# Optimization experiments

Hardware: AMD Instinct MI355X
Metric: run time of the kernel (lower is better)

## Reference

```python
import jax, jax.numpy as jnp
import numpy as np
from jax import lax

N_QUBITS = 4   # in_channels * kernel_size^2 = 1*2*2
N_LAYERS = 2
K = 2
STRIDE = 1


def _bshape(theta, N):
    # broadcast scalar or (N,) angle to (N, 1, 1, ..., 1) for statevector broadcasting
    return jnp.broadcast_to(theta, (N,)).reshape((N,) + (1,) * N_QUBITS)


def _rx(state, theta, w):
    # RX(theta) on wire w (axis w+1): cos(t/2) I - i sin(t/2) X
    N = state.shape[0]
    c = _bshape(jnp.cos(theta * 0.5), N)
    s = _bshape(jnp.sin(theta * 0.5), N)
    return c * state - 1j * s * jnp.flip(state, axis=w + 1)


def _rz(state, theta, w):
    # RZ(theta): phase e^{-i t/2} on |0>, e^{+i t/2} on |1> of wire w
    N = state.shape[0]
    sgn = jnp.array([-0.5, 0.5], dtype=state.real.dtype).reshape(
        (1,) * (w + 1) + (2,) + (1,) * (N_QUBITS - 1 - w))
    return state * jnp.exp(1j * (_bshape(theta, N) * sgn))


def _cnot(state, control, target):
    ca, ta = control + 1, target + 1
    s0 = jnp.take(state, 0, axis=ca)
    s1 = jnp.take(state, 1, axis=ca)
    ta2 = ta if ta < ca else ta - 1
    s1 = jnp.flip(s1, axis=ta2)
    return jnp.stack([s0, s1], axis=ca)


def _simulate(angles, params):
    # angles: (N, n_qubits) float32; params: (n_layers, n_qubits, 2)
    N = angles.shape[0]
    state = jnp.zeros((N,) + (2,) * N_QUBITS, dtype=jnp.complex64)
    state = state.at[(slice(None),) + (0,) * N_QUBITS].set(1.0)
    # AngleEmbedding: RX(x_w) on wire w
    for w in range(N_QUBITS):
        state = _rx(state, angles[:, w], w)
    # quantum_circuit_1
    for l in range(N_LAYERS):
        for w in range(N_QUBITS):
            state = _rx(state, params[l, w, 0], w)
            state = _rz(state, params[l, w, 1], w)
        for w in range(N_QUBITS - 1):
            # qml.CNOT(wires=[w+1, w]) -> control w+1, target w
            state = _cnot(state, w + 1, w)
    probs = state.real ** 2 + state.imag ** 2  # (N, 2,...,2)
    zs = []
    for w in range(N_QUBITS):
        other = tuple(a for a in range(1, N_QUBITS + 1) if a != w + 1)
        m = probs.sum(axis=other)  # (N, 2)
        zs.append(m[:, 0] - m[:, 1])
    return jnp.stack(zs, axis=1)  # (N, n_qubits)


def _forward(x, params):
    B, C, H, W = x.shape
    Ho = (H - K) // STRIDE + 1
    Wo = (W - K) // STRIDE + 1
    # (B, C*K*K, Ho, Wo); feature dim flattened channel-major (C, kh, kw),
    # matching torch.flatten(input[:, :, i:i+k, j:j+k], start_dim=1)
    patches = lax.conv_general_dilated_patches(x, (K, K), (STRIDE, STRIDE), 'VALID')
    angles = patches.transpose(0, 2, 3, 1).reshape(-1, N_QUBITS)  # (B*Ho*Wo, nq)
    z = _simulate(angles, params)  # (B*Ho*Wo, nq)
    return z.reshape(B, Ho, Wo, N_QUBITS).transpose(0, 3, 1, 2)  # (B, nq, Ho, Wo)


def setup_inputs() -> dict:
    key = jax.random.key(0)
    k1, k2 = jax.random.split(key)
    x = jax.random.uniform(k1, (32, 1, 128, 128), dtype=jnp.float32)
    params = jax.random.uniform(k2, (N_LAYERS, N_QUBITS, 2), dtype=jnp.float32)
    return {"x": x, "params": params}


def reference(x, params):
    return _forward(x, params)
```

## Files before the change

kernel.cpp:

```cpp
#include <hip/hip_runtime.h>


#define HH 128
#define WW 128
#define HO 127
#define WO 127
#define BB 32

template <int M>
__device__ __forceinline__ void rx_gate(float* re, float* im, float th) {
    float s, c;
    __sincosf(th * 0.5f, &s, &c);
#pragma unroll
    for (int idx = 0; idx < 16; ++idx) {
        if (idx & M) continue;
        const int p = idx | M;
        float r0 = re[idx], i0 = im[idx], r1 = re[p], i1 = im[p];
        re[idx] = fmaf(c, r0, s * i1);
        im[idx] = fmaf(c, i0, -s * r1);
        re[p]   = fmaf(c, r1, s * i0);
        im[p]   = fmaf(c, i1, -s * r0);
    }
}

template <int M>
__device__ __forceinline__ void rz_gate(float* re, float* im, float th) {
    float sp, cp;
    __sincosf(th * 0.5f, &sp, &cp);
#pragma unroll
    for (int idx = 0; idx < 16; ++idx) {
        float r = re[idx], q = im[idx];
        if (idx & M) {
            re[idx] = fmaf(r, cp, -q * sp);
            im[idx] = fmaf(q, cp, r * sp);
        } else {
            re[idx] = fmaf(r, cp, q * sp);
            im[idx] = fmaf(q, cp, -r * sp);
        }
    }
}

template <int CM, int TM>
__device__ __forceinline__ void cnot_gate(float* re, float* im) {
#pragma unroll
    for (int idx = 0; idx < 16; ++idx) {
        if ((idx & CM) && !(idx & TM)) {
            const int p = idx | TM;
            float t;
            t = re[idx]; re[idx] = re[p]; re[p] = t;
            t = im[idx]; im[idx] = im[p]; im[p] = t;
        }
    }
}

__global__ __launch_bounds__(256) void qconv_kernel(
    const float* __restrict__ x, const float* __restrict__ prm,
    float* __restrict__ out, int total) {
    int tid = blockIdx.x * blockDim.x + threadIdx.x;
    if (tid >= total) return;

    int j = tid % WO;
    int t = tid / WO;
    int i = t % HO;
    int b = t / HO;

    const float* xp = x + ((size_t)b * HH + i) * WW + j;
    float a0 = xp[0], a1 = xp[1], a2 = xp[WW], a3 = xp[WW + 1];

    float re[16], im[16];
#pragma unroll
    for (int k = 0; k < 16; ++k) { re[k] = 0.f; im[k] = 0.f; }
    re[0] = 1.0f;

    rx_gate<8>(re, im, a0);
    rx_gate<4>(re, im, a1);
    rx_gate<2>(re, im, a2);
    rx_gate<1>(re, im, a3);

#pragma unroll
    for (int l = 0; l < 2; ++l) {
        const float* p = prm + l * 8;
        rx_gate<8>(re, im, p[0]); rz_gate<8>(re, im, p[1]);
        rx_gate<4>(re, im, p[2]); rz_gate<4>(re, im, p[3]);
        rx_gate<2>(re, im, p[4]); rz_gate<2>(re, im, p[5]);
        rx_gate<1>(re, im, p[6]); rz_gate<1>(re, im, p[7]);
        cnot_gate<4, 8>(re, im);
        cnot_gate<2, 4>(re, im);
        cnot_gate<1, 2>(re, im);
    }

    float z0 = 0.f, z1 = 0.f, z2 = 0.f, z3 = 0.f;
#pragma unroll
    for (int idx = 0; idx < 16; ++idx) {
        float pr = fmaf(re[idx], re[idx], im[idx] * im[idx]);
        z0 += (idx & 8) ? -pr : pr;
        z1 += (idx & 4) ? -pr : pr;
        z2 += (idx & 2) ? -pr : pr;
        z3 += (idx & 1) ? -pr : pr;
    }

    float* o = out + (((size_t)b * 4) * HO + (size_t)i) * WO + j;
    o[0]            = z0;
    o[HO * WO]      = z1;
    o[2 * HO * WO]  = z2;
    o[3 * HO * WO]  = z3;
}

extern "C" void kernel_launch(void* const* d_in, const int* in_sizes, int n_in,
                              void* d_out, int out_size, void* d_ws, size_t ws_size,
                              hipStream_t stream) {
    const float* x = (const float*)d_in[0];
    const float* prm = (const float*)d_in[1];
    float* out = (float*)d_out;
    const int total = BB * HO * WO;
    const int blocks = (total + 255) / 256;
    qconv_kernel<<<blocks, 256, 0, stream>>>(x, prm, out, total);
}
```

Before: 75.19 us.

## Precompute Pauli-basis observable coefficients and evaluate as trig polynomial

Splits the work into a tiny setup kernel and an evaluation kernel. The setup kernel builds the 16x16 parameter unitary and expands each Z expectation into 81 coefficients over products of {1, sin, cos} of the input angles. The per-pixel kernel then evaluates that polynomial instead of simulating the full statevector through all the gates. This removes most per-thread arithmetic, but adds a second launch with a single-block serial setup and reads the coefficient table from workspace memory.

```diff
diff --git a/kernel.cpp b/kernel.cpp
--- a/kernel.cpp
+++ b/kernel.cpp
@@ -53,8 +53,80 @@
     }
 }
 
-__global__ __launch_bounds__(256) void qconv_kernel(
-    const float* __restrict__ x, const float* __restrict__ prm,
+__device__ __forceinline__ void param_circuit(float* re, float* im,
+                                              const float* __restrict__ prm) {
+#pragma unroll
+    for (int l = 0; l < 2; ++l) {
+        const float* p = prm + l * 8;
+        rx_gate<8>(re, im, p[0]); rz_gate<8>(re, im, p[1]);
+        rx_gate<4>(re, im, p[2]); rz_gate<4>(re, im, p[3]);
+        rx_gate<2>(re, im, p[4]); rz_gate<2>(re, im, p[5]);
+        rx_gate<1>(re, im, p[6]); rz_gate<1>(re, im, p[7]);
+        cnot_gate<4, 8>(re, im);
+        cnot_gate<2, 4>(re, im);
+        cnot_gate<1, 2>(re, im);
+    }
+}
+
+__global__ __launch_bounds__(384) void qconv_setup(const float* __restrict__ prm,
+                                                   float* __restrict__ W) {
+    __shared__ float Ur[16][16];
+    __shared__ float Ui[16][16];
+    const int tid = threadIdx.x;
+    if (tid < 16) {
+        float re[16], im[16];
+#pragma unroll
+        for (int k = 0; k < 16; ++k) { re[k] = (k == tid) ? 1.f : 0.f; im[k] = 0.f; }
+        param_circuit(re, im, prm);
+#pragma unroll
+        for (int k = 0; k < 16; ++k) { Ur[k][tid] = re[k]; Ui[k][tid] = im[k]; }
+    }
+    __syncthreads();
+    if (tid < 324) {
+        const int w = tid / 81;
+        int p = tid % 81;
+        const int t3 = p % 3; p /= 3;
+        const int t2 = p % 3; p /= 3;
+        const int t1 = p % 3;
+        const int t0 = p / 3;
+        const int f = (t0 == 1 ? 8 : 0) | (t1 == 1 ? 4 : 0) |
+                      (t2 == 1 ? 2 : 0) | (t3 == 1 ? 1 : 0);
+        const int zbit = 8 >> w;
+        float acc = 0.f;
+        for (int i = 0; i < 16; ++i) {
+            float pr = 1.f, pi = 0.f;
+            {
+                int ib;
+                ib = (i >> 3) & 1;
+                if (t0 == 2) { if (ib) { pr = -pr; pi = -pi; } }
+                else if (t0 == 1) { float tt = pr; if (ib) { pr = -pi; pi = tt; } else { pr = pi; pi = -tt; } }
+                ib = (i >> 2) & 1;
+                if (t1 == 2) { if (ib) { pr = -pr; pi = -pi; } }
+                else if (t1 == 1) { float tt = pr; if (ib) { pr = -pi; pi = tt; } else { pr = pi; pi = -tt; } }
+                ib = (i >> 1) & 1;
+                if (t2 == 2) { if (ib) { pr = -pr; pi = -pi; } }
+                else if (t2 == 1) { float tt = pr; if (ib) { pr = -pi; pi = tt; } else { pr = pi; pi = -tt; } }
+                ib = i & 1;
+                if (t3 == 2) { if (ib) { pr = -pr; pi = -pi; } }
+                else if (t3 == 1) { float tt = pr; if (ib) { pr = -pi; pi = tt; } else { pr = pi; pi = -tt; } }
+            }
+            const int j = i ^ f;
+            float sr = 0.f, si = 0.f;
+            for (int k = 0; k < 16; ++k) {
+                float zk = (k & zbit) ? -1.f : 1.f;
+                float ar = Ur[k][j], ai = Ui[k][j];
+                float br = Ur[k][i], bi = Ui[k][i];
+                sr += zk * fmaf(ar, br, ai * bi);
+                si += zk * fmaf(ar, bi, -ai * br);
+            }
+            acc += pr * sr - pi * si;
+        }
+        W[tid] = acc * (1.0f / 16.0f);
+    }
+}
+
+__global__ __launch_bounds__(256) void qconv_eval(
+    const float* __restrict__ x, const float* __restrict__ W,
     float* __restrict__ out, int total) {
     int tid = blockIdx.x * blockDim.x + threadIdx.x;
     if (tid >= total) return;
@@ -67,43 +139,48 @@
     const float* xp = x + ((size_t)b * HH + i) * WW + j;
     float a0 = xp[0], a1 = xp[1], a2 = xp[WW], a3 = xp[WW + 1];
 
-    float re[16], im[16];
+    float s0, c0, s1, c1, s2, c2, s3, c3;
+    __sincosf(a0, &s0, &c0);
+    __sincosf(a1, &s1, &c1);
+    __sincosf(a2, &s2, &c2);
+    __sincosf(a3, &s3, &c3);
+    const float y0 = -s0, y1 = -s1, y2 = -s2, y3 = -s3;
+
+    float z[4];
 #pragma unroll
-    for (int k = 0; k < 16; ++k) { re[k] = 0.f; im[k] = 0.f; }
-    re[0] = 1.0f;
-
-    rx_gate<8>(re, im, a0);
-    rx_gate<4>(re, im, a1);
-    rx_gate<2>(re, im, a2);
-    rx_gate<1>(re, im, a3);
-
+    for (int w = 0; w < 4; ++w) {
+        const float* Ww = W + w * 81;
+        float accw = 0.f;
 #pragma unroll
-    for (int l = 0; l < 2; ++l) {
-        const float* p = prm + l * 8;
-        rx_gate<8>(re, im, p[0]); rz_gate<8>(re, im, p[1]);
-        rx_gate<4>(re, im, p[2]); rz_gate<4>(re, im, p[3]);
-        rx_gate<2>(re, im, p[4]); rz_gate<2>(re, im, p[5]);
-        rx_gate<1>(re, im, p[6]); rz_gate<1>(re, im, p[7]);
-        cnot_gate<4, 8>(re, im);
-        cnot_gate<2, 4>(re, im);
-        cnot_gate<1, 2>(re, im);
-    }
-
-    float z0 = 0.f, z1 = 0.f, z2 = 0.f, z3 = 0.f;
+        for (int p0 = 0; p0 < 3; ++p0) {
+            float b0 = 0.f;
 #pragma unroll
-    for (int idx = 0; idx < 16; ++idx) {
-        float pr = fmaf(re[idx], re[idx], im[idx] * im[idx]);
-        z0 += (idx & 8) ? -pr : pr;
-        z1 += (idx & 4) ? -pr : pr;
-        z2 += (idx & 2) ? -pr : pr;
-        z3 += (idx & 1) ? -pr : pr;
+            for (int p1 = 0; p1 < 3; ++p1) {
+                float b1 = 0.f;
+#pragma unroll
+                for (int p2 = 0; p2 < 3; ++p2) {
+                    const float* q = Ww + ((p0 * 3 + p1) * 3 + p2) * 3;
+                    float d = fmaf(c3, q[2], fmaf(y3, q[1], q[0]));
+                    if (p2 == 0)      b1 += d;
+                    else if (p2 == 1) b1 = fmaf(y2, d, b1);
+                    else              b1 = fmaf(c2, d, b1);
+                }
+                if (p1 == 0)      b0 += b1;
+                else if (p1 == 1) b0 = fmaf(y1, b1, b0);
+                else              b0 = fmaf(c1, b1, b0);
+            }
+            if (p0 == 0)      accw += b0;
+            else if (p0 == 1) accw = fmaf(y0, b0, accw);
+            else              accw = fmaf(c0, b0, accw);
+        }
+        z[w] = accw;
     }
 
     float* o = out + (((size_t)b * 4) * HO + (size_t)i) * WO + j;
-    o[0]            = z0;
-    o[HO * WO]      = z1;
-    o[2 * HO * WO]  = z2;
-    o[3 * HO * WO]  = z3;
+    o[0]           = z[0];
+    o[HO * WO]     = z[1];
+    o[2 * HO * WO] = z[2];
+    o[3 * HO * WO] = z[3];
 }
 
 extern "C" void kernel_launch(void* const* d_in, const int* in_sizes, int n_in,
@@ -112,7 +189,11 @@
     const float* x = (const float*)d_in[0];
     const float* prm = (const float*)d_in[1];
     float* out = (float*)d_out;
+    float* W = (float*)d_ws;
+
+    qconv_setup<<<1, 384, 0, stream>>>(prm, W);
+
     const int total = BB * HO * WO;
     const int blocks = (total + 255) / 256;
-    qconv_kernel<<<blocks, 256, 0, stream>>>(x, prm, out, total);
+    qconv_eval<<<blocks, 256, 0, stream>>>(x, W, out, total);
 }
```

After: 77.76 us. +3.4%, slower.
